# Performance work log

Hardware: AMD Instinct MI355X
Metric: run time of the kernel (lower is better)

## Reference

```python
import jax, jax.numpy as jnp
import numpy as np

B, S, D = 16, 2048, 256
SCALE = 1.0 / np.sqrt(D).astype(np.float32)

def setup_inputs() -> dict:
    key = jax.random.key(0)
    k1, k2, k3, k4 = jax.random.split(key, 4)
    x = jax.random.normal(k1, (B, S, D), dtype=jnp.float32)
    w_qkv = jax.random.normal(k2, (3 * D, D), dtype=jnp.float32) * (1.0 / np.sqrt(D))
    w_out = jax.random.normal(k3, (D, D), dtype=jnp.float32) * (1.0 / np.sqrt(D))
    b_out = jax.random.normal(k4, (D,), dtype=jnp.float32) * 0.01
    return {"x": x, "w_qkv": w_qkv, "w_out": w_out, "b_out": b_out}

def reference(x, w_qkv, w_out, b_out):
    # qkv: [B, S, 3D] = x @ W_qkv^T (torch Linear convention)
    qkv = jnp.einsum('bsd,ed->bse', x, w_qkv)
    q, k, v = jnp.split(qkv, 3, axis=-1)  # each [B, S, D]
    scores = jnp.einsum('bsd,btd->bst', q, k) * SCALE  # [B, S, S]
    attn = jax.nn.softmax(scores, axis=-1)  # dropout = identity (eval mode)
    ctx = jnp.einsum('bst,btd->bsd', attn, v)  # [B, S, D]
    out = jnp.einsum('bsd,ed->bse', ctx, w_out) + b_out
    return out
```

## Files before the change

kernel.cpp:

```cpp
#include <hip/hip_runtime.h>
#include <hip/hip_bf16.h>


typedef short bf16x8 __attribute__((ext_vector_type(8)));
typedef float f32x4 __attribute__((ext_vector_type(4)));

#define MFMA16(a, b, c) __builtin_amdgcn_mfma_f32_16x16x32_bf16((a), (b), (c), 0, 0, 0)

__device__ __forceinline__ unsigned short f2bf(float f) {
  unsigned int x;
  __builtin_memcpy(&x, &f, 4);
  x = x + 0x7fffu + ((x >> 16) & 1u);
  return (unsigned short)(x >> 16);
}
__device__ __forceinline__ unsigned int pack2(float a, float b) {
  float2 t;
  t.x = a;
  t.y = b;
  __hip_bfloat162 h = __float22bfloat162_rn(t);
  unsigned int u;
  __builtin_memcpy(&u, &h, 4);
  return u;
}

typedef __attribute__((address_space(3))) void as3_void;
typedef __attribute__((address_space(1))) const void as1_void;
__device__ __forceinline__ void gl_lds16(const void* g, void* l) {
  __builtin_amdgcn_global_load_lds((as1_void*)(unsigned long long)g,
                                   (as3_void*)(unsigned int)(unsigned long long)l,
                                   16, 0, 0);
}

__global__ __launch_bounds__(512, 1) void qkv_kernel(
    const float* __restrict__ X, const float* __restrict__ W,
    unsigned short* __restrict__ Q, unsigned short* __restrict__ Kp,
    unsigned short* __restrict__ Vt) {
  __shared__ unsigned short Al[128 * 256];
  __shared__ unsigned short Bl[128 * 256];
  const int m0 = blockIdx.x * 128;
  const int t = threadIdx.x;
  const int w = t >> 6, lane = t & 63, lo = lane & 15, quad = lane >> 4;
  const int wr = (w >> 2) * 64, wc = (w & 3) * 32;

#pragma unroll
  for (int r = 0; r < 8; ++r) {
    int ci = r * 512 + t;
    int row = ci >> 5, c = ci & 31;
    int s = (c & 24) | ((c ^ (row & 7)) & 7);
    const float* xp = X + (size_t)(m0 + row) * 256 + c * 8;
    float4 a0 = *(const float4*)xp, a1 = *(const float4*)(xp + 4);
    uint4 ua;
    ua.x = pack2(a0.x, a0.y);
    ua.y = pack2(a0.z, a0.w);
    ua.z = pack2(a1.x, a1.y);
    ua.w = pack2(a1.z, a1.w);
    *(uint4*)(&Al[row * 256 + s * 8]) = ua;
  }

  for (int n = 0; n < 6; ++n) {
    const int n0 = n * 128;
    if (n > 0) __syncthreads();
#pragma unroll
    for (int r = 0; r < 8; ++r) {
      int ci = r * 512 + t;
      int row = ci >> 5, c = ci & 31;
      int s = (c & 24) | ((c ^ (row & 7)) & 7);
      const float* wp = W + (size_t)(n0 + row) * 256 + c * 8;
      float4 b0 = *(const float4*)wp, b1 = *(const float4*)(wp + 4);
      uint4 ub;
      ub.x = pack2(b0.x, b0.y);
      ub.y = pack2(b0.z, b0.w);
      ub.z = pack2(b1.x, b1.y);
      ub.w = pack2(b1.z, b1.w);
      *(uint4*)(&Bl[row * 256 + s * 8]) = ub;
    }
    __syncthreads();

    f32x4 zero4 = {0.f, 0.f, 0.f, 0.f};
    f32x4 acc[4][2];
#pragma unroll
    for (int i = 0; i < 4; i++)
#pragma unroll
      for (int j = 0; j < 2; j++) acc[i][j] = zero4;

#pragma unroll
    for (int kc = 0; kc < 8; ++kc) {
      const int c = kc * 4 + quad;
      const int jj = (c & 24) | ((c ^ (lo & 7)) & 7);
      bf16x8 af[4], bfr[2];
#pragma unroll
      for (int mt = 0; mt < 4; ++mt)
        af[mt] = *(const bf16x8*)(&Al[(wr + mt * 16 + lo) * 256 + jj * 8]);
#pragma unroll
      for (int nt = 0; nt < 2; ++nt)
        bfr[nt] = *(const bf16x8*)(&Bl[(wc + nt * 16 + lo) * 256 + jj * 8]);
#pragma unroll
      for (int mt = 0; mt < 4; ++mt)
#pragma unroll
        for (int nt = 0; nt < 2; ++nt)
          acc[mt][nt] = MFMA16(af[mt], bfr[nt], acc[mt][nt]);
    }

    const int mb = m0 + wr, nb = n0 + wc;
    if (n0 < 256) {
#pragma unroll
      for (int mt = 0; mt < 4; ++mt)
#pragma unroll
        for (int nt = 0; nt < 2; ++nt) {
          int m = mb + mt * 16 + quad * 4;
          int nn = nb + nt * 16 + lo;
          unsigned short* p = Q + (size_t)m * 256 + nn;
          p[0] = f2bf(acc[mt][nt][0]);
          p[256] = f2bf(acc[mt][nt][1]);
          p[512] = f2bf(acc[mt][nt][2]);
          p[768] = f2bf(acc[mt][nt][3]);
        }
    } else if (n0 < 512) {
#pragma unroll
      for (int mt = 0; mt < 4; ++mt)
#pragma unroll
        for (int nt = 0; nt < 2; ++nt) {
          int m = mb + mt * 16 + quad * 4;
          int nn = nb + nt * 16 + lo - 256;
          unsigned short* p = Kp + (size_t)m * 256 + nn;
          p[0] = f2bf(acc[mt][nt][0]);
          p[256] = f2bf(acc[mt][nt][1]);
          p[512] = f2bf(acc[mt][nt][2]);
          p[768] = f2bf(acc[mt][nt][3]);
        }
    } else {
#pragma unroll
      for (int mt = 0; mt < 4; ++mt)
#pragma unroll
        for (int nt = 0; nt < 2; ++nt) {
          int m = mb + mt * 16 + quad * 4;
          int d = nb + nt * 16 + lo - 512;
          int b = m >> 11, s = m & 2047;
          uint2 v;
          v.x = pack2(acc[mt][nt][0], acc[mt][nt][1]);
          v.y = pack2(acc[mt][nt][2], acc[mt][nt][3]);
          *(uint2*)(Vt + ((size_t)(b * 256 + d)) * 2048 + s) = v;
        }
    }
  }
}

__global__ __launch_bounds__(512, 2) void attn_kernel(
    const unsigned short* __restrict__ Q, const unsigned short* __restrict__ K,
    const unsigned short* __restrict__ Vt, unsigned short* __restrict__ C) {
  __shared__ __attribute__((aligned(16))) unsigned short smem[65536];
  const int id = blockIdx.x;
  const int b = id & 15;
  const int qt = id >> 4;
  const int t = threadIdx.x;
  const int w = t >> 6, lane = t & 63, lo = lane & 15, quad = lane >> 4;
  constexpr float SCALE_LOG2E = 0.0625f * 1.4426950408889634f;

  const unsigned short* Kb = K + (size_t)b * 2048 * 256;
  const unsigned short* Vb = Vt + (size_t)b * 256 * 2048;

  unsigned int gkoff[4], gvoff[4];
  int loK[4], loV[4];
#pragma unroll
  for (int r = 0; r < 4; ++r) {
    int ck = r * 512 + t;
    int row = ck >> 5, j = ck & 31;
    int srcj = (j & 16) | ((j ^ (row & 15)) & 15);
    gkoff[r] = (unsigned int)((row * 256 + srcj * 8) * 2);
    loK[r] = __builtin_amdgcn_readfirstlane((r * 512 + w * 64) * 8);

    int cv = r * 512 + t;
    int d = cv >> 3, slot = cv & 7;
    int g = slot ^ (d & 7);
    gvoff[r] = (unsigned int)((d * 2048 + g * 8) * 2);
    loV[r] = __builtin_amdgcn_readfirstlane(16384 + (r * 512 + w * 64) * 8);
  }

  const int qrow = b * 2048 + qt * 128 + w * 16 + lo;
  const unsigned short* qp = Q + (size_t)qrow * 256;
  bf16x8 qf[8];
#pragma unroll
  for (int ks = 0; ks < 8; ++ks)
    qf[ks] = *(const bf16x8*)(qp + ks * 32 + quad * 8);

  f32x4 zero4 = {0.f, 0.f, 0.f, 0.f};
  f32x4 oacc[16];
#pragma unroll
  for (int i = 0; i < 16; i++) oacc[i] = zero4;
  float m_run = -1e30f, l_run = 0.f;

#pragma unroll
  for (int r = 0; r < 4; ++r) {
    gl_lds16((const char*)Kb + gkoff[r], &smem[loK[r]]);
    gkoff[r] += 64 * 256 * 2;
  }
#pragma unroll
  for (int r = 0; r < 4; ++r) {
    gl_lds16((const char*)Vb + gvoff[r], &smem[loV[r]]);
    gvoff[r] += 64 * 2;
  }

  for (int it = 0; it < 32; ++it) {
    asm volatile("s_waitcnt vmcnt(0)" ::: "memory");
    __syncthreads();
    if (it < 31) {
      const int pn = ((it + 1) & 1) * 32768;
#pragma unroll
      for (int r = 0; r < 4; ++r) {
        gl_lds16((const char*)Kb + gkoff[r], &smem[pn + loK[r]]);
        gkoff[r] += 64 * 256 * 2;
      }
#pragma unroll
      for (int r = 0; r < 4; ++r) {
        gl_lds16((const char*)Vb + gvoff[r], &smem[pn + loV[r]]);
        gvoff[r] += 64 * 2;
      }
    }
    const unsigned short* Kl = smem + (it & 1) * 32768;
    const unsigned short* Vl = Kl + 16384;

    f32x4 sacc[4];
#pragma unroll
    for (int r = 0; r < 4; ++r) sacc[r] = zero4;
    __builtin_amdgcn_s_setprio(1);
#pragma unroll
    for (int ks = 0; ks < 8; ++ks) {
      const int c = ks * 4 + quad;
      const int jj = (c & 16) | ((c ^ lo) & 15);
#pragma unroll
      for (int r = 0; r < 4; ++r) {
        bf16x8 kf = *(const bf16x8*)(&Kl[(r * 16 + lo) * 256 + jj * 8]);
        sacc[r] = MFMA16(kf, qf[ks], sacc[r]);
      }
    }
    __builtin_amdgcn_s_setprio(0);

    float p[4][4];
    float cmax = -1e30f;
#pragma unroll
    for (int r = 0; r < 4; r++)
#pragma unroll
      for (int i = 0; i < 4; i++) {
        p[r][i] = sacc[r][i] * SCALE_LOG2E;
        cmax = fmaxf(cmax, p[r][i]);
      }
    cmax = fmaxf(cmax, __shfl_xor(cmax, 16));
    cmax = fmaxf(cmax, __shfl_xor(cmax, 32));
    if (!__all(cmax <= m_run + 8.f)) {
      float mnew = fmaxf(m_run, cmax);
      float alpha = exp2f(m_run - mnew);
      l_run *= alpha;
#pragma unroll
      for (int i = 0; i < 16; i++) oacc[i] *= alpha;
      m_run = mnew;
    }
    float rsum = 0.f;
#pragma unroll
    for (int r = 0; r < 4; r++)
#pragma unroll
      for (int i = 0; i < 4; i++) {
        p[r][i] = exp2f(p[r][i] - m_run);
        rsum += p[r][i];
      }
    rsum += __shfl_xor(rsum, 16);
    rsum += __shfl_xor(rsum, 32);
    l_run += rsum;

    unsigned int pk[4][2];
#pragma unroll
    for (int r = 0; r < 4; r++) {
      pk[r][0] = pack2(p[r][0], p[r][1]);
      pk[r][1] = pack2(p[r][2], p[r][3]);
    }

#pragma unroll
    for (int ks2 = 0; ks2 < 2; ++ks2) {
      union {
        unsigned int u[4];
        bf16x8 v;
      } cvt;
#pragma unroll
      for (int dd = 0; dd < 4; ++dd) {
        int src = lo + 16 * ((2 * quad + (dd >> 1)) & 3);
        unsigned int v0 = (unsigned int)__shfl((int)pk[2 * ks2][dd & 1], src);
        unsigned int v1 = (unsigned int)__shfl((int)pk[2 * ks2 + 1][dd & 1], src);
        cvt.u[dd] = (quad >> 1) ? v1 : v0;
      }
      bf16x8 pf = cvt.v;
      __builtin_amdgcn_s_setprio(1);
#pragma unroll
      for (int dt = 0; dt < 16; ++dt) {
        int slot = (ks2 * 4 + quad) ^ (lo & 7);
        bf16x8 vf = *(const bf16x8*)(&Vl[(dt * 16 + lo) * 64 + slot * 8]);
        oacc[dt] = MFMA16(vf, pf, oacc[dt]);
      }
      __builtin_amdgcn_s_setprio(0);
    }
  }

  float inv = 1.0f / l_run;
  unsigned short* cp = C + (size_t)qrow * 256;
#pragma unroll
  for (int dt = 0; dt < 16; ++dt) {
    uint2 v;
    v.x = pack2(oacc[dt][0] * inv, oacc[dt][1] * inv);
    v.y = pack2(oacc[dt][2] * inv, oacc[dt][3] * inv);
    *(uint2*)(cp + dt * 16 + quad * 4) = v;
  }
}

__global__ __launch_bounds__(512, 1) void proj_kernel(
    const unsigned short* __restrict__ Xc, const float* __restrict__ W,
    const float* __restrict__ bias, float* __restrict__ out) {
  __shared__ unsigned short Al[128 * 256];
  __shared__ unsigned short Bl[128 * 256];
  const int m0 = blockIdx.x * 128;
  const int t = threadIdx.x;
  const int w = t >> 6, lane = t & 63, lo = lane & 15, quad = lane >> 4;
  const int wr = (w >> 2) * 64, wc = (w & 3) * 32;

  const unsigned short* Xb = Xc + (size_t)m0 * 256;
#pragma unroll
  for (int r = 0; r < 8; ++r) {
    int idx = r * 512 + t;
    int row = idx >> 5, sc = idx & 31;
    int c = (sc & 24) | ((sc ^ (row & 7)) & 7);
    int lofs = __builtin_amdgcn_readfirstlane((r * 512 + w * 64) * 8);
    gl_lds16(Xb + (size_t)row * 256 + c * 8, &Al[lofs]);
  }

  for (int n = 0; n < 2; ++n) {
    const int n0 = n * 128;
    if (n > 0) __syncthreads();
#pragma unroll
    for (int r = 0; r < 8; ++r) {
      int ci = r * 512 + t;
      int row = ci >> 5, c = ci & 31;
      int s = (c & 24) | ((c ^ (row & 7)) & 7);
      const float* wp = W + (size_t)(n0 + row) * 256 + c * 8;
      float4 b0 = *(const float4*)wp, b1 = *(const float4*)(wp + 4);
      uint4 ub;
      ub.x = pack2(b0.x, b0.y);
      ub.y = pack2(b0.z, b0.w);
      ub.z = pack2(b1.x, b1.y);
      ub.w = pack2(b1.z, b1.w);
      *(uint4*)(&Bl[row * 256 + s * 8]) = ub;
    }
    if (n == 0) asm volatile("s_waitcnt vmcnt(0)" ::: "memory");
    __syncthreads();

    f32x4 zero4 = {0.f, 0.f, 0.f, 0.f};
    f32x4 acc[4][2];
#pragma unroll
    for (int i = 0; i < 4; i++)
#pragma unroll
      for (int j = 0; j < 2; j++) acc[i][j] = zero4;

#pragma unroll
    for (int kc = 0; kc < 8; ++kc) {
      const int c = kc * 4 + quad;
      const int jj = (c & 24) | ((c ^ (lo & 7)) & 7);
      bf16x8 af[4], bfr[2];
#pragma unroll
      for (int mt = 0; mt < 4; ++mt)
        af[mt] = *(const bf16x8*)(&Al[(wr + mt * 16 + lo) * 256 + jj * 8]);
#pragma unroll
      for (int nt = 0; nt < 2; ++nt)
        bfr[nt] = *(const bf16x8*)(&Bl[(wc + nt * 16 + lo) * 256 + jj * 8]);
#pragma unroll
      for (int mt = 0; mt < 4; ++mt)
#pragma unroll
        for (int nt = 0; nt < 2; ++nt)
          acc[mt][nt] = MFMA16(af[mt], bfr[nt], acc[mt][nt]);
    }

    const int mb = m0 + wr, nb = n0 + wc;
#pragma unroll
    for (int nt = 0; nt < 2; ++nt) {
      int nn = nb + nt * 16 + lo;
      float bv = bias[nn];
#pragma unroll
      for (int mt = 0; mt < 4; ++mt) {
        int m = mb + mt * 16 + quad * 4;
        float* p = out + (size_t)m * 256 + nn;
        p[0] = acc[mt][nt][0] + bv;
        p[256] = acc[mt][nt][1] + bv;
        p[512] = acc[mt][nt][2] + bv;
        p[768] = acc[mt][nt][3] + bv;
      }
    }
  }
}

extern "C" void kernel_launch(void* const* d_in, const int* in_sizes, int n_in,
                              void* d_out, int out_size, void* d_ws, size_t ws_size,
                              hipStream_t stream) {
  const float* X = (const float*)d_in[0];
  const float* Wq = (const float*)d_in[1];
  const float* Wo = (const float*)d_in[2];
  const float* Bo = (const float*)d_in[3];
  float* out = (float*)d_out;
  unsigned short* ws = (unsigned short*)d_ws;

  const size_t NE = (size_t)16 * 2048 * 256;
  unsigned short* Qb = ws;
  unsigned short* Kb = ws + NE;
  unsigned short* Vt = ws + 2 * NE;
  unsigned short* Cx = ws;

  qkv_kernel<<<dim3(256), 512, 0, stream>>>(X, Wq, Qb, Kb, Vt);
  attn_kernel<<<dim3(256), 512, 0, stream>>>(Qb, Kb, Vt, Cx);
  proj_kernel<<<dim3(256), 512, 0, stream>>>(Cx, Wo, Bo, out);
}
```

Baseline: 214.7 us.

## Switch attention to 32x32 MFMA with split-KV across wave halves

Rewrites the attention inner loop to use 32x32x16 bf16 MFMA instead of 16x16x32. Each group of four waves now owns a 32-query tile, and the two wave halves each take a different 32-key half of every KV block. The halves keep separate online-softmax states and merge them through LDS at the end. This aims to cut LDS fragment loads and cross-lane shuffles per MFMA and to raise MFMA efficiency. It adds a final cross-wave reduction, two accumulator chains for the score dot product, and bf16 rounding of the partial output that goes through LDS.

```diff
diff --git a/kernel.cpp b/kernel.cpp
--- a/kernel.cpp
+++ b/kernel.cpp
@@ -4,8 +4,10 @@
 
 typedef short bf16x8 __attribute__((ext_vector_type(8)));
 typedef float f32x4 __attribute__((ext_vector_type(4)));
+typedef float f32x16 __attribute__((ext_vector_type(16)));
 
 #define MFMA16(a, b, c) __builtin_amdgcn_mfma_f32_16x16x32_bf16((a), (b), (c), 0, 0, 0)
+#define MFMA32(a, b, c) __builtin_amdgcn_mfma_f32_32x32x16_bf16((a), (b), (c), 0, 0, 0)
 
 __device__ __forceinline__ unsigned short f2bf(float f) {
   unsigned int x;
@@ -21,6 +23,12 @@
   unsigned int u;
   __builtin_memcpy(&u, &h, 4);
   return u;
+}
+__device__ __forceinline__ float bfu2f(unsigned int lo16) {
+  unsigned int v = lo16 << 16;
+  float f;
+  __builtin_memcpy(&f, &v, 4);
+  return f;
 }
 
 typedef __attribute__((address_space(3))) void as3_void;
@@ -153,7 +161,8 @@
   const int b = id & 15;
   const int qt = id >> 4;
   const int t = threadIdx.x;
-  const int w = t >> 6, lane = t & 63, lo = lane & 15, quad = lane >> 4;
+  const int w = t >> 6, lane = t & 63, lq = lane & 31, hi = lane >> 5;
+  const int hh = w >> 2, qg = w & 3;
   constexpr float SCALE_LOG2E = 0.0625f * 1.4426950408889634f;
 
   const unsigned short* Kb = K + (size_t)b * 2048 * 256;
@@ -164,29 +173,28 @@
 #pragma unroll
   for (int r = 0; r < 4; ++r) {
     int ck = r * 512 + t;
-    int row = ck >> 5, j = ck & 31;
-    int srcj = (j & 16) | ((j ^ (row & 15)) & 15);
-    gkoff[r] = (unsigned int)((row * 256 + srcj * 8) * 2);
+    int krow = ck >> 5, kc = ck & 31;
+    int ksrc = kc ^ (krow & 31);
+    gkoff[r] = (unsigned int)((krow * 256 + ksrc * 8) * 2);
     loK[r] = __builtin_amdgcn_readfirstlane((r * 512 + w * 64) * 8);
 
     int cv = r * 512 + t;
-    int d = cv >> 3, slot = cv & 7;
-    int g = slot ^ (d & 7);
-    gvoff[r] = (unsigned int)((d * 2048 + g * 8) * 2);
+    int vd = cv >> 3, vs = cv & 7;
+    int vsrc = vs ^ (vd & 7);
+    gvoff[r] = (unsigned int)((vd * 2048 + vsrc * 8) * 2);
     loV[r] = __builtin_amdgcn_readfirstlane(16384 + (r * 512 + w * 64) * 8);
   }
 
-  const int qrow = b * 2048 + qt * 128 + w * 16 + lo;
+  const int qrow = b * 2048 + qt * 128 + qg * 32 + lq;
   const unsigned short* qp = Q + (size_t)qrow * 256;
-  bf16x8 qf[8];
-#pragma unroll
-  for (int ks = 0; ks < 8; ++ks)
-    qf[ks] = *(const bf16x8*)(qp + ks * 32 + quad * 8);
-
-  f32x4 zero4 = {0.f, 0.f, 0.f, 0.f};
-  f32x4 oacc[16];
-#pragma unroll
-  for (int i = 0; i < 16; i++) oacc[i] = zero4;
+  bf16x8 qf[16];
+#pragma unroll
+  for (int st = 0; st < 16; ++st)
+    qf[st] = *(const bf16x8*)(qp + st * 16 + hi * 8);
+
+  f32x16 oacc[8];
+#pragma unroll
+  for (int i = 0; i < 8; i++) oacc[i] = 0.f;
   float m_run = -1e30f, l_run = 0.f;
 
 #pragma unroll
@@ -219,93 +227,133 @@
     const unsigned short* Kl = smem + (it & 1) * 32768;
     const unsigned short* Vl = Kl + 16384;
 
-    f32x4 sacc[4];
-#pragma unroll
-    for (int r = 0; r < 4; ++r) sacc[r] = zero4;
+    f32x16 s0 = 0.f, s1 = 0.f;
     __builtin_amdgcn_s_setprio(1);
 #pragma unroll
-    for (int ks = 0; ks < 8; ++ks) {
-      const int c = ks * 4 + quad;
-      const int jj = (c & 16) | ((c ^ lo) & 15);
-#pragma unroll
-      for (int r = 0; r < 4; ++r) {
-        bf16x8 kf = *(const bf16x8*)(&Kl[(r * 16 + lo) * 256 + jj * 8]);
-        sacc[r] = MFMA16(kf, qf[ks], sacc[r]);
-      }
+    for (int st = 0; st < 16; ++st) {
+      const int slot = (st * 2 + hi) ^ lq;
+      bf16x8 kf = *(const bf16x8*)(&Kl[(hh * 32 + lq) * 256 + slot * 8]);
+      if (st & 1)
+        s1 = MFMA32(kf, qf[st], s1);
+      else
+        s0 = MFMA32(kf, qf[st], s0);
     }
     __builtin_amdgcn_s_setprio(0);
 
-    float p[4][4];
+    float p[16];
     float cmax = -1e30f;
 #pragma unroll
-    for (int r = 0; r < 4; r++)
-#pragma unroll
-      for (int i = 0; i < 4; i++) {
-        p[r][i] = sacc[r][i] * SCALE_LOG2E;
-        cmax = fmaxf(cmax, p[r][i]);
-      }
-    cmax = fmaxf(cmax, __shfl_xor(cmax, 16));
+    for (int i = 0; i < 16; i++) {
+      p[i] = (s0[i] + s1[i]) * SCALE_LOG2E;
+      cmax = fmaxf(cmax, p[i]);
+    }
     cmax = fmaxf(cmax, __shfl_xor(cmax, 32));
     if (!__all(cmax <= m_run + 8.f)) {
       float mnew = fmaxf(m_run, cmax);
       float alpha = exp2f(m_run - mnew);
       l_run *= alpha;
 #pragma unroll
-      for (int i = 0; i < 16; i++) oacc[i] *= alpha;
+      for (int i = 0; i < 8; i++) oacc[i] *= alpha;
       m_run = mnew;
     }
     float rsum = 0.f;
 #pragma unroll
-    for (int r = 0; r < 4; r++)
-#pragma unroll
-      for (int i = 0; i < 4; i++) {
-        p[r][i] = exp2f(p[r][i] - m_run);
-        rsum += p[r][i];
-      }
-    rsum += __shfl_xor(rsum, 16);
+    for (int i = 0; i < 16; i++) {
+      p[i] = exp2f(p[i] - m_run);
+      rsum += p[i];
+    }
     rsum += __shfl_xor(rsum, 32);
     l_run += rsum;
 
-    unsigned int pk[4][2];
-#pragma unroll
-    for (int r = 0; r < 4; r++) {
-      pk[r][0] = pack2(p[r][0], p[r][1]);
-      pk[r][1] = pack2(p[r][2], p[r][3]);
-    }
-
-#pragma unroll
-    for (int ks2 = 0; ks2 < 2; ++ks2) {
+    {
+      unsigned int x0 = pack2(p[0], p[1]), x1 = pack2(p[2], p[3]);
+      unsigned int y0 = pack2(p[4], p[5]), y1 = pack2(p[6], p[7]);
+      unsigned int ex0 = (unsigned int)__shfl_xor((int)x0, 32);
+      unsigned int ex1 = (unsigned int)__shfl_xor((int)x1, 32);
+      unsigned int ey0 = (unsigned int)__shfl_xor((int)y0, 32);
+      unsigned int ey1 = (unsigned int)__shfl_xor((int)y1, 32);
       union {
         unsigned int u[4];
         bf16x8 v;
       } cvt;
-#pragma unroll
-      for (int dd = 0; dd < 4; ++dd) {
-        int src = lo + 16 * ((2 * quad + (dd >> 1)) & 3);
-        unsigned int v0 = (unsigned int)__shfl((int)pk[2 * ks2][dd & 1], src);
-        unsigned int v1 = (unsigned int)__shfl((int)pk[2 * ks2 + 1][dd & 1], src);
-        cvt.u[dd] = (quad >> 1) ? v1 : v0;
-      }
+      cvt.u[0] = hi ? ey0 : x0;
+      cvt.u[1] = hi ? ey1 : x1;
+      cvt.u[2] = hi ? y0 : ex0;
+      cvt.u[3] = hi ? y1 : ex1;
       bf16x8 pf = cvt.v;
       __builtin_amdgcn_s_setprio(1);
 #pragma unroll
-      for (int dt = 0; dt < 16; ++dt) {
-        int slot = (ks2 * 4 + quad) ^ (lo & 7);
-        bf16x8 vf = *(const bf16x8*)(&Vl[(dt * 16 + lo) * 64 + slot * 8]);
-        oacc[dt] = MFMA16(vf, pf, oacc[dt]);
+      for (int dt = 0; dt < 8; ++dt) {
+        const int slot = (hh * 4 + hi) ^ (lq & 7);
+        bf16x8 vf = *(const bf16x8*)(&Vl[(dt * 32 + lq) * 64 + slot * 8]);
+        oacc[dt] = MFMA32(vf, pf, oacc[dt]);
       }
       __builtin_amdgcn_s_setprio(0);
     }
-  }
-
-  float inv = 1.0f / l_run;
-  unsigned short* cp = C + (size_t)qrow * 256;
-#pragma unroll
-  for (int dt = 0; dt < 16; ++dt) {
-    uint2 v;
-    v.x = pack2(oacc[dt][0] * inv, oacc[dt][1] * inv);
-    v.y = pack2(oacc[dt][2] * inv, oacc[dt][3] * inv);
-    *(uint2*)(cp + dt * 16 + quad * 4) = v;
+    {
+      unsigned int z0 = pack2(p[8], p[9]), z1 = pack2(p[10], p[11]);
+      unsigned int w0 = pack2(p[12], p[13]), w1 = pack2(p[14], p[15]);
+      unsigned int ez0 = (unsigned int)__shfl_xor((int)z0, 32);
+      unsigned int ez1 = (unsigned int)__shfl_xor((int)z1, 32);
+      unsigned int ew0 = (unsigned int)__shfl_xor((int)w0, 32);
+      unsigned int ew1 = (unsigned int)__shfl_xor((int)w1, 32);
+      union {
+        unsigned int u[4];
+        bf16x8 v;
+      } cvt;
+      cvt.u[0] = hi ? ew0 : z0;
+      cvt.u[1] = hi ? ew1 : z1;
+      cvt.u[2] = hi ? w0 : ez0;
+      cvt.u[3] = hi ? w1 : ez1;
+      bf16x8 pf = cvt.v;
+      __builtin_amdgcn_s_setprio(1);
+#pragma unroll
+      for (int dt = 0; dt < 8; ++dt) {
+        const int slot = (hh * 4 + 2 + hi) ^ (lq & 7);
+        bf16x8 vf = *(const bf16x8*)(&Vl[(dt * 32 + lq) * 64 + slot * 8]);
+        oacc[dt] = MFMA32(vf, pf, oacc[dt]);
+      }
+      __builtin_amdgcn_s_setprio(0);
+    }
+  }
+
+  __syncthreads();
+  float* st = (float*)smem;
+  if (hi == 0) {
+    st[w * 32 + lq] = m_run;
+    st[256 + w * 32 + lq] = l_run;
+  }
+  __syncthreads();
+  float m_o = st[(w ^ 4) * 32 + lq];
+  float l_o = st[256 + (w ^ 4) * 32 + lq];
+  float m_tot = fmaxf(m_run, m_o);
+  float f_self = exp2f(m_run - m_tot);
+  float l_tot = l_run * f_self + l_o * exp2f(m_o - m_tot);
+  unsigned short* Of = smem + 1024;
+  if (hh == 1) {
+#pragma unroll
+    for (int dt = 0; dt < 8; ++dt)
+#pragma unroll
+      for (int i = 0; i < 16; i += 2) {
+        int d = dt * 32 + (i & 3) + 8 * (i >> 2) + 4 * hi;
+        *(unsigned int*)&Of[qg * 8448 + lq * 264 + d] =
+            pack2(oacc[dt][i] * f_self, oacc[dt][i + 1] * f_self);
+      }
+  }
+  __syncthreads();
+  if (hh == 0) {
+    float inv = 1.0f / l_tot;
+    unsigned short* cp = C + (size_t)qrow * 256;
+#pragma unroll
+    for (int dt = 0; dt < 8; ++dt)
+#pragma unroll
+      for (int i = 0; i < 16; i += 2) {
+        int d = dt * 32 + (i & 3) + 8 * (i >> 2) + 4 * hi;
+        unsigned int u = *(unsigned int*)&Of[qg * 8448 + lq * 264 + d];
+        float o0 = oacc[dt][i] * f_self + bfu2f(u & 0xffffu);
+        float o1 = oacc[dt][i + 1] * f_self + bfu2f(u >> 16);
+        *(unsigned int*)(cp + d) = pack2(o0 * inv, o1 * inv);
+      }
   }
 }
 
```

Measured after the change: 242.3 us. +12.9%, slower.
